# Performance work log

Hardware: AMD Instinct MI355X
Metric: run time of the kernel (lower is better)

Reference implementation:

```python
import jax, jax.numpy as jnp
jax.config.update("jax_enable_x64", True)
import numpy as np

# Dimensions from init_kwargs
B = 1024            # batch of binarized input patterns
T = 4096            # total_input_bits
N = 4096            # num_neurons
NB = 16             # n_bits_per_neuron
MEM_SIZE = 1 << NB  # 65536 addressable cells per neuron
BITS_PER_CELL = 2
CELLS_PER_WORD = 62 // BITS_PER_CELL          # 31
WPN = (MEM_SIZE + CELLS_PER_WORD - 1) // CELLS_PER_WORD  # 2115 words per neuron


def setup_inputs() -> dict:
    key = jax.random.key(0)
    k1, k2, k3 = jax.random.split(key, 3)
    # binarized input patterns in {0,1}
    x = jax.random.randint(k1, (B, T), 0, 2, dtype=jnp.int32)
    # per-neuron connections into the input bit vector
    connections = jax.random.randint(k2, (N, NB), 0, T, dtype=jnp.int64)
    # bit-packed 2-bit RAM cells (trained state); random words stand in for a
    # trained memory -- the read math is identical regardless of contents
    memory_words = jax.random.randint(k3, (N, WPN), 0, 2**31 - 1, dtype=jnp.int64)
    return {"x": x, "connections": connections, "memory_words": memory_words}


def reference(x, connections, memory_words):
    # Gather each neuron's connected input bits: [B, N, NB]
    bits = jnp.take(x, connections, axis=1).astype(jnp.int64)
    # MSB-first address decode (matches binary_addresses = 2**arange(NB-1,-1,-1))
    weights = (jnp.int64(1) << jnp.arange(NB - 1, -1, -1, dtype=jnp.int64))
    addr = jnp.sum(bits * weights, axis=-1)  # [B, N] in [0, MEM_SIZE)
    # _cell_coords: locate the packed 2-bit cell
    word_index = addr // CELLS_PER_WORD          # [B, N]
    bit_shift = (addr % CELLS_PER_WORD) * BITS_PER_CELL
    # Irregular gather of the packed words: memory_words[n, word_index[b, n]]
    words = memory_words[jnp.arange(N, dtype=jnp.int64)[None, :], word_index]  # [B, N]
    # _read_cells: extract 2-bit cell value in {0,1,2} (FALSE, TRUE, EMPTY)
    vals = (words >> bit_shift) & 3
    return vals
```

## Files before the change

### kernel.cpp

```cpp
#include <hip/hip_runtime.h>
#include <stdint.h>

constexpr int Tdim = 4096;
constexpr int Ndim = 4096;
constexpr int Bdim = 1024;
constexpr int NB   = 16;
constexpr int WPN  = 2115;

__device__ __forceinline__ int probe_stride(const int* __restrict__ p) {
    const int l = threadIdx.x & 63;
    return (__ballot(p[2 * l + 1] == 0) == ~0ull) ? 2 : 1;
}

__global__ __launch_bounds__(256) void pack_kernel(const int* __restrict__ x,
                                                   uint32_t* __restrict__ xT) {
    const int sx = probe_stride(x);
    const int t  = blockIdx.x * 256 + threadIdx.x;
    const int bg = blockIdx.y;
    uint32_t w = 0;
#pragma unroll
    for (int bl = 0; bl < 32; ++bl) {
        const size_t idx = ((size_t)(bg * 32 + bl) * Tdim + t) * sx;
        w |= (uint32_t)(x[idx] & 1) << bl;
    }
    xT[(size_t)bg * Tdim + t] = w;
}

__global__ __launch_bounds__(256) void row_kernel(const uint32_t* __restrict__ xT,
                                                  const int* __restrict__ conn,
                                                  const int* __restrict__ mem,
                                                  int* __restrict__ out) {
    const int sc = probe_stride(conn);
    const int sm = probe_stride(mem);

    const int i  = blockIdx.x;
    const int bx = (i & 255) * 8 + (i >> 8);
    const int n0 = bx * 2;

    const int tid = threadIdx.x;

    __shared__ uint32_t rowbuf[2 * WPN];
    __shared__ uint32_t bits[2 * 32 * 16];
    __shared__ uint64_t omask[2][16][2];

    const size_t base = (size_t)n0 * WPN;
    if (sm == 2) {
        const uint2* m2 = (const uint2*)mem;
#pragma unroll
        for (int k = 0; k < 17; ++k) {
            const int idx = k * 256 + tid;
            if (idx < 2 * WPN) rowbuf[idx] = m2[base + idx].x;
        }
    } else {
        const uint32_t* m1 = (const uint32_t*)mem;
#pragma unroll
        for (int k = 0; k < 17; ++k) {
            const int idx = k * 256 + tid;
            if (idx < 2 * WPN) rowbuf[idx] = m1[base + idx];
        }
    }

#pragma unroll
    for (int k = 0; k < 4; ++k) {
        const int idx = k * 256 + tid;
        const int n_l = idx >> 9;
        const int bg  = (idx >> 4) & 31;
        const int j   = idx & 15;
        const int c   = conn[((n0 + n_l) * NB + j) * sc];
        bits[idx] = xT[(size_t)bg * Tdim + c];
    }
    __syncthreads();

    const int w   = tid >> 6;
    const int l   = tid & 63;
    const int bit = l & 31;
    const int hi  = l >> 5;
#pragma unroll
    for (int n_l = 0; n_l < 2; ++n_l) {
        const uint32_t* myrow = &rowbuf[n_l * WPN];
        const uint32_t* myb   = &bits[n_l * 512];
#pragma unroll
        for (int it = 0; it < 4; ++it) {
            const int bg = w * 8 + it * 2 + hi;
            const uint32_t* bp = &myb[bg * 16];
            uint32_t addr = 0;
#pragma unroll
            for (int j = 0; j < 16; ++j)
                addr = (addr << 1) | ((bp[j] >> bit) & 1u);
            const uint32_t wi = addr / 31u;
            const uint32_t sh = (addr - wi * 31u) * 2u;
            const uint32_t v = (uint32_t)(((uint64_t)myrow[wi] >> sh) & 3ull);
            const uint64_t b0 = __ballot((v & 1u) != 0u);
            const uint64_t b1 = __ballot((v & 2u) != 0u);
            if (l == 0) {
                omask[n_l][w * 4 + it][0] = b0;
                omask[n_l][w * 4 + it][1] = b1;
            }
        }
    }
    __syncthreads();

#pragma unroll
    for (int k = 0; k < 8; ++k) {
        const int t2  = k * 256 + tid;
        const int n_l = t2 & 1;
        const int b   = t2 >> 1;
        const uint64_t m0 = omask[n_l][b >> 6][0];
        const uint64_t m1 = omask[n_l][b >> 6][1];
        const int s = b & 63;
        const int v = (int)((m0 >> s) & 1ull) | ((int)((m1 >> s) & 1ull) << 1);
        out[(size_t)b * Ndim + n0 + n_l] = v;
    }
}

__global__ __launch_bounds__(256) void direct_kernel(const int* __restrict__ x,
                                                     const int* __restrict__ conn,
                                                     const int* __restrict__ mem,
                                                     int* __restrict__ out) {
    const int sx = probe_stride(x);
    const int sc = probe_stride(conn);
    const int sm = probe_stride(mem);
    const int n  = blockIdx.x * 256 + threadIdx.x;
    const int b  = blockIdx.y;
    const int* cp = conn + (size_t)n * NB * sc;
    const int* xr = x + (size_t)b * Tdim * sx;
    uint32_t addr = 0;
#pragma unroll
    for (int j = 0; j < 16; ++j)
        addr = (addr << 1) | (uint32_t)(xr[(size_t)cp[j * sc] * sx] & 1);
    const uint32_t wi = addr / 31u;
    const uint32_t sh = (addr - wi * 31u) * 2u;
    const uint64_t wd = (uint32_t)mem[((size_t)n * WPN + wi) * sm];
    out[(size_t)b * Ndim + n] = (int)((wd >> sh) & 3u);
}

extern "C" void kernel_launch(void* const* d_in, const int* in_sizes, int n_in,
                              void* d_out, int out_size, void* d_ws, size_t ws_size,
                              hipStream_t stream) {
    const int* x    = (const int*)d_in[0];
    const int* conn = (const int*)d_in[1];
    const int* mem  = (const int*)d_in[2];
    int*       out  = (int*)d_out;
    uint32_t*  xT   = (uint32_t*)d_ws;

    const size_t need = (size_t)(Bdim / 32) * Tdim * sizeof(uint32_t);
    if (ws_size >= need) {
        dim3 g1(Tdim / 256, Bdim / 32);
        pack_kernel<<<g1, 256, 0, stream>>>(x, xT);
        row_kernel<<<Ndim / 2, 256, 0, stream>>>(xT, conn, mem, out);
    } else {
        dim3 g3(Ndim / 256, Bdim);
        direct_kernel<<<g3, 256, 0, stream>>>(x, conn, mem, out);
    }
}
```

Baseline: 125.3 us.

## Split output unpack into separate kernel with bitmask intermediate

The row kernel now writes compact per-neuron ballot bitmasks to a workspace buffer instead of scattering 8-byte-wide int writes across the output. A new unpack kernel reads the masks for 16 neurons per block and writes the output so that each row gets 64-byte contiguous segments, which is meant to improve write coalescing. Shared-memory address bits are also read as uint4 vectors. This adds an extra kernel launch and a small intermediate buffer round trip, and it needs more workspace, so it can fall back to the direct path if the workspace is too small.

```diff
diff --git a/kernel.cpp b/kernel.cpp
--- a/kernel.cpp
+++ b/kernel.cpp
@@ -29,19 +29,17 @@
 __global__ __launch_bounds__(256) void row_kernel(const uint32_t* __restrict__ xT,
                                                   const int* __restrict__ conn,
                                                   const int* __restrict__ mem,
-                                                  int* __restrict__ out) {
+                                                  uint64_t* __restrict__ pmask) {
     const int sc = probe_stride(conn);
     const int sm = probe_stride(mem);
 
-    const int i  = blockIdx.x;
-    const int bx = (i & 255) * 8 + (i >> 8);
-    const int n0 = bx * 2;
-
+    const int n0  = blockIdx.x * 2;
     const int tid = threadIdx.x;
 
     __shared__ uint32_t rowbuf[2 * WPN];
-    __shared__ uint32_t bits[2 * 32 * 16];
-    __shared__ uint64_t omask[2][16][2];
+    __shared__ uint4    bits4[2 * 32 * 4];
+    __shared__ uint64_t omask[2 * 16 * 2];
+    uint32_t* bits = (uint32_t*)bits4;
 
     const size_t base = (size_t)n0 * WPN;
     if (sm == 2) {
@@ -78,38 +76,61 @@
 #pragma unroll
     for (int n_l = 0; n_l < 2; ++n_l) {
         const uint32_t* myrow = &rowbuf[n_l * WPN];
-        const uint32_t* myb   = &bits[n_l * 512];
 #pragma unroll
         for (int it = 0; it < 4; ++it) {
             const int bg = w * 8 + it * 2 + hi;
-            const uint32_t* bp = &myb[bg * 16];
+            const uint4* bp4 = &bits4[n_l * 128 + bg * 4];
+            uint32_t wv[16];
+#pragma unroll
+            for (int q = 0; q < 4; ++q) {
+                const uint4 v4 = bp4[q];
+                wv[q * 4 + 0] = v4.x; wv[q * 4 + 1] = v4.y;
+                wv[q * 4 + 2] = v4.z; wv[q * 4 + 3] = v4.w;
+            }
             uint32_t addr = 0;
 #pragma unroll
             for (int j = 0; j < 16; ++j)
-                addr = (addr << 1) | ((bp[j] >> bit) & 1u);
+                addr = (addr << 1) | ((wv[j] >> bit) & 1u);
             const uint32_t wi = addr / 31u;
             const uint32_t sh = (addr - wi * 31u) * 2u;
             const uint32_t v = (uint32_t)(((uint64_t)myrow[wi] >> sh) & 3ull);
             const uint64_t b0 = __ballot((v & 1u) != 0u);
             const uint64_t b1 = __ballot((v & 2u) != 0u);
             if (l == 0) {
-                omask[n_l][w * 4 + it][0] = b0;
-                omask[n_l][w * 4 + it][1] = b1;
+                omask[n_l * 32 + (w * 4 + it) * 2 + 0] = b0;
+                omask[n_l * 32 + (w * 4 + it) * 2 + 1] = b1;
             }
         }
     }
     __syncthreads();
 
+    if (tid < 64) pmask[(size_t)n0 * 32 + tid] = omask[tid];
+}
+
+__global__ __launch_bounds__(256) void unpack_kernel(const uint64_t* __restrict__ pmask,
+                                                     int* __restrict__ out) {
+    const int n0  = blockIdx.x * 16;
+    const int tid = threadIdx.x;
+
+    __shared__ uint64_t m[16 * 32];
 #pragma unroll
-    for (int k = 0; k < 8; ++k) {
-        const int t2  = k * 256 + tid;
-        const int n_l = t2 & 1;
-        const int b   = t2 >> 1;
-        const uint64_t m0 = omask[n_l][b >> 6][0];
-        const uint64_t m1 = omask[n_l][b >> 6][1];
+    for (int k = 0; k < 2; ++k) {
+        const int idx = k * 256 + tid;
+        m[idx] = pmask[(size_t)n0 * 32 + idx];
+    }
+    __syncthreads();
+
+    const int nl = tid & 15;
+    const int b0 = tid >> 4;
+#pragma unroll
+    for (int q = 0; q < 64; ++q) {
+        const int b = q * 16 + b0;
+        const int p = b >> 6;
         const int s = b & 63;
+        const uint64_t m0 = m[nl * 32 + p * 2 + 0];
+        const uint64_t m1 = m[nl * 32 + p * 2 + 1];
         const int v = (int)((m0 >> s) & 1ull) | ((int)((m1 >> s) & 1ull) << 1);
-        out[(size_t)b * Ndim + n0 + n_l] = v;
+        out[(size_t)b * Ndim + n0 + nl] = v;
     }
 }
 
@@ -142,12 +163,14 @@
     const int* mem  = (const int*)d_in[2];
     int*       out  = (int*)d_out;
     uint32_t*  xT   = (uint32_t*)d_ws;
+    uint64_t*  pmask = (uint64_t*)((char*)d_ws + (size_t)(Bdim / 32) * Tdim * 4);
 
-    const size_t need = (size_t)(Bdim / 32) * Tdim * sizeof(uint32_t);
+    const size_t need = (size_t)(Bdim / 32) * Tdim * 4 + (size_t)Ndim * 32 * 8;
     if (ws_size >= need) {
         dim3 g1(Tdim / 256, Bdim / 32);
         pack_kernel<<<g1, 256, 0, stream>>>(x, xT);
-        row_kernel<<<Ndim / 2, 256, 0, stream>>>(xT, conn, mem, out);
+        row_kernel<<<Ndim / 2, 256, 0, stream>>>(xT, conn, mem, pmask);
+        unpack_kernel<<<Ndim / 16, 256, 0, stream>>>(pmask, out);
     } else {
         dim3 g3(Ndim / 256, Bdim);
         direct_kernel<<<g3, 256, 0, stream>>>(x, conn, mem, out);
```

Result: faster. 106.6 us (-14.9%).
